# Kernel tuning notes

Measured on AMD Instinct MI355X. Metric: run time of the kernel, lower is better.

## Reference

```python
import jax, jax.numpy as jnp
import numpy as np

B = 256          # number of trees
DEPTH = 8        # complete binary tree depth -> 9 levels
M = 2 ** (DEPTH + 1) - 1   # 511 nodes per tree
N = B * M        # 130816 total nodes
X_SIZE = 128
H_SIZE = 128


def _build_forest():
    j = np.arange(M)
    parent_local = np.maximum((j - 1) // 2, 0)
    lvl = np.array([int(x + 1).bit_length() - 1 for x in j], dtype=np.int32)
    off = (np.arange(B) * M).astype(np.int32)
    parent = (parent_local[None, :] + off[:, None]).reshape(-1).astype(np.int32)
    level = np.tile(lvl, B)
    tree_id = np.repeat(np.arange(B, dtype=np.int32), M)
    isleaf = (level == DEPTH)
    jj = j[1:]
    edge_src = (jj[None, :] + off[:, None]).reshape(-1).astype(np.int32)   # child
    edge_dst = parent[edge_src]                                            # parent
    return parent, level, tree_id, isleaf, edge_src, edge_dst, off


def setup_inputs() -> dict:
    key = jax.random.key(0)
    ks = jax.random.split(key, 12)
    _, level, tree_id, isleaf, edge_src, edge_dst, root_ids = _build_forest()
    sx = 1.0 / np.sqrt(X_SIZE)
    sh = 1.0 / np.sqrt(H_SIZE)
    sxh = 1.0 / np.sqrt(X_SIZE + H_SIZE)
    inp = {
        "X": jax.random.normal(ks[0], (N, X_SIZE), dtype=jnp.float32),
        "h0": jnp.zeros((N, H_SIZE), jnp.float32),
        "c0": jnp.zeros((N, H_SIZE), jnp.float32),
        # bottom-up cell params
        "W_iou_bu": jax.random.normal(ks[1], (3 * H_SIZE, X_SIZE), dtype=jnp.float32) * sx,
        "U_iou_bu": jax.random.normal(ks[2], (3 * H_SIZE, H_SIZE), dtype=jnp.float32) * sh,
        "b_iou_bu": jnp.zeros((1, 3 * H_SIZE), jnp.float32),
        "Uf_bu": jax.random.normal(ks[3], (H_SIZE, H_SIZE), dtype=jnp.float32) * sh,
        "bf_bu": jax.random.normal(ks[4], (H_SIZE,), dtype=jnp.float32) * sh,
        # top-down cell params (x_size = X_SIZE + H_SIZE)
        "W_iou_td": jax.random.normal(ks[5], (3 * H_SIZE, X_SIZE + H_SIZE), dtype=jnp.float32) * sxh,
        "U_iou_td": jax.random.normal(ks[6], (3 * H_SIZE, H_SIZE), dtype=jnp.float32) * sh,
        "b_iou_td": jnp.zeros((1, 3 * H_SIZE), jnp.float32),
        "Uf_td": jax.random.normal(ks[7], (H_SIZE, H_SIZE), dtype=jnp.float32) * sh,
        "bf_td": jax.random.normal(ks[8], (H_SIZE,), dtype=jnp.float32) * sh,
        # graph structure
        "edge_src": jnp.asarray(edge_src),
        "edge_dst": jnp.asarray(edge_dst),
        "level": jnp.asarray(level),
        "tree_id": jnp.asarray(tree_id),
        "isleaf": jnp.asarray(isleaf),
        "root_ids": jnp.asarray(root_ids),
    }
    return inp


def _propagate(X_in, W_iou, U_iou, b_iou, Uf, bf, src, dst, level, no_in, h0, c0, order):
    """Level-synchronous ChildSum TreeLSTM propagation (== dgl.prop_nodes_topo)."""
    n = X_in.shape[0]
    WX = X_in @ W_iou.T                                   # [N, 3H]
    h, c = h0, c0
    for t in order:
        h_src = h[src]                                    # [E, H] gather child/parent states
        c_src = c[src]
        h_tild = jax.ops.segment_sum(h_src, dst, num_segments=n)
        f = jax.nn.sigmoid(h_src @ Uf.T + bf)             # per-edge forget gate
        c_red = jax.ops.segment_sum(f * c_src, dst, num_segments=n)
        iou = WX + h_tild @ U_iou.T + b_iou
        i, o, u = jnp.split(iou, 3, axis=1)
        c_base = jnp.where(no_in[:, None], c0, c_red)     # frontier nodes with no in-edges keep init c
        c_new = jax.nn.sigmoid(i) * jnp.tanh(u) + c_base
        h_new = jax.nn.sigmoid(o) * jnp.tanh(c_new)
        m = (level == t)[:, None]                          # only commit current topological level
        h = jnp.where(m, h_new, h)
        c = jnp.where(m, c_new, c)
    return h


def reference(X, h0, c0, W_iou_bu, U_iou_bu, b_iou_bu, Uf_bu, bf_bu,
              W_iou_td, U_iou_td, b_iou_td, Uf_td, bf_td,
              edge_src, edge_dst, level, tree_id, isleaf, root_ids):
    # bottom-up: messages flow child -> parent, leaves first
    h_bu = _propagate(X, W_iou_bu, U_iou_bu, b_iou_bu, Uf_bu, bf_bu,
                      edge_src, edge_dst, level, isleaf, h0, c0,
                      order=range(DEPTH, -1, -1))
    # top-down: reversed edges, root first
    X_td = jnp.concatenate([X, h_bu], axis=1)
    h_td = _propagate(X_td, W_iou_td, U_iou_td, b_iou_td, Uf_td, bf_td,
                      edge_dst, edge_src, level, level == 0, h0, c0,
                      order=range(0, DEPTH + 1))
    root_h_bottom_up = h_bu[root_ids]                     # [B, H]
    leaf = isleaf.astype(h_td.dtype)
    sums = jax.ops.segment_sum(h_td * leaf[:, None], tree_id, num_segments=root_ids.shape[0])
    cnt = jax.ops.segment_sum(leaf, tree_id, num_segments=root_ids.shape[0])
    leaves_h_top_down = sums / cnt[:, None]               # per-tree mean over leaves
    return jnp.concatenate([root_h_bottom_up, leaves_h_top_down], axis=1)
```

## Files before the change

kernel.cpp:

```cpp
#include <hip/hip_runtime.h>
#include <cmath>

#define NTREE 256
#define MPT 511
#define NNODE (NTREE * MPT)
#define HS 128

typedef __bf16 bf16x8 __attribute__((ext_vector_type(8)));
typedef float  f32x4  __attribute__((ext_vector_type(4)));

__device__ __forceinline__ float sigf(float x) {
  float e = __builtin_amdgcn_exp2f(x * -1.44269504f);
  return __builtin_amdgcn_rcpf(1.0f + e);
}
__device__ __forceinline__ float tanh_fast(float x) {
  float e = __builtin_amdgcn_exp2f(x * -2.88539008f);
  return __builtin_amdgcn_rcpf(1.0f + e) * 2.0f - 1.0f;
}
__device__ __forceinline__ f32x4 mm(bf16x8 a, bf16x8 b, f32x4 c) {
  return __builtin_amdgcn_mfma_f32_16x16x32_bf16(a, b, c, 0, 0, 0);
}
__device__ __forceinline__ int swz(int row, int rb, int kb) { return row * rb + (kb ^ ((row & 7) << 4)); }
__device__ __forceinline__ void st8(char* s, int row, int rb, int chunk, bf16x8 v) {
  *reinterpret_cast<bf16x8*>(s + swz(row, rb, chunk * 16)) = v;
}
__device__ __forceinline__ bf16x8 ld8(const char* s, int row, int rb, int kb) {
  return *reinterpret_cast<const bf16x8*>(s + swz(row, rb, kb));
}
__device__ __forceinline__ bf16x8 g8(const __bf16* p) { return *reinterpret_cast<const bf16x8*>(p); }
__device__ __forceinline__ bf16x8 gx8(const float* p) {
  float4 v0 = reinterpret_cast<const float4*>(p)[0];
  float4 v1 = reinterpret_cast<const float4*>(p)[1];
  bf16x8 o;
  o[0] = (__bf16)v0.x; o[1] = (__bf16)v0.y; o[2] = (__bf16)v0.z; o[3] = (__bf16)v0.w;
  o[4] = (__bf16)v1.x; o[5] = (__bf16)v1.y; o[6] = (__bf16)v1.z; o[7] = (__bf16)v1.w;
  return o;
}
__device__ __forceinline__ void stbf(char* s, int row, int rb, int kbyte, float v) {
  *reinterpret_cast<__bf16*>(s + row * rb + (kbyte ^ ((row & 7) << 4))) = (__bf16)v;
}

__global__ void __launch_bounds__(512, 2)
bu_bottom(const float* __restrict__ Xf,
          const __bf16* __restrict__ W, const float* __restrict__ bp,
          const __bf16* __restrict__ Uf, const float* __restrict__ bf_,
          __bf16* __restrict__ h_bu, float* __restrict__ cws)
{
  __shared__ __align__(16) char sX8[64 * 256];
  __shared__ __align__(16) char sX7[32 * 256];
  __shared__ __align__(16) char sT [32 * 256];
  __shared__ float sCr[32][128];

  const int tid = threadIdx.x, w = tid >> 6, l = tid & 63, lr = l & 15, lk = l >> 4;
  const int ch = w * 16 + lr;
  const int vb = blockIdx.x * 32;
  const int b  = vb >> 7;
  const int j7 = 127 + (vb & 127);
  const size_t g7  = (size_t)b * MPT + j7;
  const size_t gLf = (size_t)b * MPT + 2 * j7 + 1;
  const size_t gp6 = (size_t)b * MPT + ((j7 - 1) >> 1);

#pragma unroll
  for (int it = 0; it < 2; ++it) {
    int idx = tid + it * 512, n = idx >> 4, e = idx & 15;
    st8(sX8, n, 256, e, gx8(Xf + (gLf + n) * HS + e * 8));
  }
  { int n = tid >> 4, e = tid & 15;
    st8(sX7, n, 256, e, gx8(Xf + (g7 + n) * HS + e * 8)); }

  const float bia = bp[ch], boa = bp[ch + 128], bua = bp[ch + 256], bfa = bf_[ch];
  bf16x8 Uff[4];
#pragma unroll
  for (int ks = 0; ks < 4; ++ks) Uff[ks] = g8(Uf + (size_t)ch * HS + ks * 32 + lk * 8);
  __syncthreads();

  bf16x8 Bb[3][3];
  auto ldB = [&](int ks, int s) {
#pragma unroll
    for (int g2 = 0; g2 < 3; ++g2)
      Bb[s][g2] = g8(W + (size_t)(g2 * 128 + ch) * 256 + ks * 32 + lk * 8);
  };

  f32x4 acc[3][4];
#pragma unroll
  for (int g2 = 0; g2 < 3; ++g2)
#pragma unroll
    for (int mf = 0; mf < 4; ++mf) acc[g2][mf] = 0.0f;

  ldB(0, 0); ldB(1, 1);
#pragma unroll
  for (int ks = 0; ks < 4; ++ks) {
    if (ks + 2 < 4) ldB(ks + 2, (ks + 2) % 3);
    const int kb = ks * 64 + lk * 16;
    bf16x8 A0 = ld8(sX8, lr,      256, kb);
    bf16x8 A1 = ld8(sX8, 16 + lr, 256, kb);
    bf16x8 A2 = ld8(sX8, 32 + lr, 256, kb);
    bf16x8 A3 = ld8(sX8, 48 + lr, 256, kb);
#pragma unroll
    for (int g2 = 0; g2 < 3; ++g2) {
      acc[g2][0] = mm(A0, Bb[ks % 3][g2], acc[g2][0]);
      acc[g2][1] = mm(A1, Bb[ks % 3][g2], acc[g2][1]);
      acc[g2][2] = mm(A2, Bb[ks % 3][g2], acc[g2][2]);
      acc[g2][3] = mm(A3, Bb[ks % 3][g2], acc[g2][3]);
    }
  }
  float cnv[4][4], hnv[4][4];
#pragma unroll
  for (int mf = 0; mf < 4; ++mf)
#pragma unroll
    for (int j = 0; j < 4; ++j) {
      const int nrow = 16 * mf + lk * 4 + j;
      float cn = sigf(acc[0][mf][j] + bia) * tanh_fast(acc[2][mf][j] + bua);
      float hn = sigf(acc[1][mf][j] + boa) * tanh_fast(cn);
      cnv[mf][j] = cn; hnv[mf][j] = hn;
      h_bu[(gLf + nrow) * HS + ch] = (__bf16)hn;
    }
  __syncthreads();
#pragma unroll
  for (int mf = 0; mf < 4; ++mf)
#pragma unroll
    for (int j = 0; j < 4; ++j)
      stbf(sX8, 16 * mf + lk * 4 + j, 256, 2 * ch, hnv[mf][j]);
  __syncthreads();
  {
    f32x4 fa[4];
#pragma unroll
    for (int mf = 0; mf < 4; ++mf) fa[mf] = 0.0f;
#pragma unroll
    for (int ks = 0; ks < 4; ++ks) {
      const int kb = ks * 64 + lk * 16;
      fa[0] = mm(ld8(sX8, lr,      256, kb), Uff[ks], fa[0]);
      fa[1] = mm(ld8(sX8, 16 + lr, 256, kb), Uff[ks], fa[1]);
      fa[2] = mm(ld8(sX8, 32 + lr, 256, kb), Uff[ks], fa[2]);
      fa[3] = mm(ld8(sX8, 48 + lr, 256, kb), Uff[ks], fa[3]);
    }
#pragma unroll
    for (int mf = 0; mf < 4; ++mf)
#pragma unroll
      for (int p = 0; p < 2; ++p) {
        const int er = 16 * mf + lk * 4 + 2 * p;
        const int pr = er >> 1;
        float f0 = sigf(fa[mf][2 * p]     + bfa) * cnv[mf][2 * p];
        float f1 = sigf(fa[mf][2 * p + 1] + bfa) * cnv[mf][2 * p + 1];
        sCr[pr][ch] = f0 + f1;
        stbf(sT, pr, 256, 2 * ch, hnv[mf][2 * p] + hnv[mf][2 * p + 1]);
      }
  }
  __syncthreads();

  f32x4 ac2[3][2];
#pragma unroll
  for (int g2 = 0; g2 < 3; ++g2) { ac2[g2][0] = 0.0f; ac2[g2][1] = 0.0f; }
  ldB(0, 0); ldB(1, 1);
#pragma unroll
  for (int ks = 0; ks < 8; ++ks) {
    if (ks + 2 < 8) ldB(ks + 2, (ks + 2) % 3);
    const int kb = (ks & 3) * 64 + lk * 16;
    bf16x8 A0 = (ks < 4) ? ld8(sX7, lr,      256, kb) : ld8(sT, lr,      256, kb);
    bf16x8 A1 = (ks < 4) ? ld8(sX7, 16 + lr, 256, kb) : ld8(sT, 16 + lr, 256, kb);
#pragma unroll
    for (int g2 = 0; g2 < 3; ++g2) {
      ac2[g2][0] = mm(A0, Bb[ks % 3][g2], ac2[g2][0]);
      ac2[g2][1] = mm(A1, Bb[ks % 3][g2], ac2[g2][1]);
    }
  }
  float cn2[2][4], hn2[2][4];
#pragma unroll
  for (int mf = 0; mf < 2; ++mf)
#pragma unroll
    for (int j = 0; j < 4; ++j) {
      const int nr = 16 * mf + lk * 4 + j;
      float cn = sigf(ac2[0][mf][j] + bia) * tanh_fast(ac2[2][mf][j] + bua) + sCr[nr][ch];
      float hn = sigf(ac2[1][mf][j] + boa) * tanh_fast(cn);
      cn2[mf][j] = cn; hn2[mf][j] = hn;
      h_bu[(g7 + nr) * HS + ch] = (__bf16)hn;
    }
  __syncthreads();
#pragma unroll
  for (int mf = 0; mf < 2; ++mf)
#pragma unroll
    for (int j = 0; j < 4; ++j)
      stbf(sX7, 16 * mf + lk * 4 + j, 256, 2 * ch, hn2[mf][j]);
  __syncthreads();
  {
    f32x4 fb[2]; fb[0] = 0.0f; fb[1] = 0.0f;
#pragma unroll
    for (int ks = 0; ks < 4; ++ks) {
      const int kb = ks * 64 + lk * 16;
      fb[0] = mm(ld8(sX7, lr,      256, kb), Uff[ks], fb[0]);
      fb[1] = mm(ld8(sX7, 16 + lr, 256, kb), Uff[ks], fb[1]);
    }
#pragma unroll
    for (int mf = 0; mf < 2; ++mf)
#pragma unroll
      for (int p = 0; p < 2; ++p) {
        const int er = 16 * mf + lk * 4 + 2 * p;
        const size_t gp = gp6 + (er >> 1);
        float f0 = sigf(fb[mf][2 * p]     + bfa) * cn2[mf][2 * p];
        float f1 = sigf(fb[mf][2 * p + 1] + bfa) * cn2[mf][2 * p + 1];
        cws[gp * HS + ch] = f0 + f1;
        h_bu[gp * HS + ch] = (__bf16)(hn2[mf][2 * p] + hn2[mf][2 * p + 1]);
      }
  }
}

__global__ void __launch_bounds__(512, 2)
td_bottom(const float* __restrict__ Xf,
          const __bf16* __restrict__ W, const float* __restrict__ bp,
          const __bf16* __restrict__ Uf, const float* __restrict__ bf_,
          const __bf16* __restrict__ h_bu, const __bf16* __restrict__ h_td,
          const float* __restrict__ cws, float* __restrict__ part)
{
  __shared__ __align__(16) char sA7[32 * 768];
  __shared__ __align__(16) char sXH[64 * 512];
  __shared__ __align__(16) char sTd[32 * 256];
  __shared__ float sFc[32][128];

  const int tid = threadIdx.x, w = tid >> 6, l = tid & 63, lr = l & 15, lk = l >> 4;
  const int ch = w * 16 + lr;
  const int vb = blockIdx.x * 32;
  const int b  = vb >> 7;
  const int j7 = 127 + (vb & 127);
  const size_t g7  = (size_t)b * MPT + j7;
  const size_t gLf = (size_t)b * MPT + 2 * j7 + 1;
  const size_t gp6 = (size_t)b * MPT + ((j7 - 1) >> 1);

  { int n = tid >> 4, e = tid & 15;
    st8(sA7, n, 768, e,      gx8(Xf   + (g7 + n) * HS + e * 8));
    st8(sA7, n, 768, 16 + e, g8(h_bu + (g7 + n) * HS + e * 8));
    st8(sA7, n, 768, 32 + e, g8(h_td + (gp6 + (n >> 1)) * HS + e * 8)); }
#pragma unroll
  for (int it = 0; it < 2; ++it) {
    int idx = tid + it * 512, n = idx >> 4, e = idx & 15;
    st8(sXH, n, 512, e,      gx8(Xf   + (gLf + n) * HS + e * 8));
    st8(sXH, n, 512, 16 + e, g8(h_bu + (gLf + n) * HS + e * 8));
  }
  float cb[2][4];
#pragma unroll
  for (int mf = 0; mf < 2; ++mf)
#pragma unroll
    for (int j = 0; j < 4; ++j) {
      const int nr = 16 * mf + lk * 4 + j;
      cb[mf][j] = cws[(gp6 + (nr >> 1)) * HS + ch];
    }
  const float bia = bp[ch], boa = bp[ch + 128], bua = bp[ch + 256], bfa = bf_[ch];
  bf16x8 Uff[4];
#pragma unroll
  for (int ks = 0; ks < 4; ++ks) Uff[ks] = g8(Uf + (size_t)ch * HS + ks * 32 + lk * 8);
  __syncthreads();

  bf16x8 Bb[3][3];
  auto ldB = [&](int ks, int s) {
#pragma unroll
    for (int g2 = 0; g2 < 3; ++g2)
      Bb[s][g2] = g8(W + (size_t)(g2 * 128 + ch) * 384 + ks * 32 + lk * 8);
  };

  f32x4 ac[3][2];
#pragma unroll
  for (int g2 = 0; g2 < 3; ++g2) { ac[g2][0] = 0.0f; ac[g2][1] = 0.0f; }
  ldB(0, 0); ldB(1, 1);
#pragma unroll
  for (int ks = 0; ks < 12; ++ks) {
    if (ks + 2 < 12) ldB(ks + 2, (ks + 2) % 3);
    const int kb = ks * 64 + lk * 16;
    bf16x8 A0 = ld8(sA7, lr,      768, kb);
    bf16x8 A1 = ld8(sA7, 16 + lr, 768, kb);
#pragma unroll
    for (int g2 = 0; g2 < 3; ++g2) {
      ac[g2][0] = mm(A0, Bb[ks % 3][g2], ac[g2][0]);
      ac[g2][1] = mm(A1, Bb[ks % 3][g2], ac[g2][1]);
    }
  }
  float cn7[2][4];
#pragma unroll
  for (int mf = 0; mf < 2; ++mf)
#pragma unroll
    for (int j = 0; j < 4; ++j) {
      const int nr = 16 * mf + lk * 4 + j;
      float cn = sigf(ac[0][mf][j] + bia) * tanh_fast(ac[2][mf][j] + bua) + cb[mf][j];
      float hn = sigf(ac[1][mf][j] + boa) * tanh_fast(cn);
      cn7[mf][j] = cn;
      stbf(sTd, nr, 256, 2 * ch, hn);
    }
  __syncthreads();
  {
    f32x4 fa[2]; fa[0] = 0.0f; fa[1] = 0.0f;
#pragma unroll
    for (int ks = 0; ks < 4; ++ks) {
      const int kb = ks * 64 + lk * 16;
      fa[0] = mm(ld8(sTd, lr,      256, kb), Uff[ks], fa[0]);
      fa[1] = mm(ld8(sTd, 16 + lr, 256, kb), Uff[ks], fa[1]);
    }
#pragma unroll
    for (int mf = 0; mf < 2; ++mf)
#pragma unroll
      for (int j = 0; j < 4; ++j) {
        const int nr = 16 * mf + lk * 4 + j;
        sFc[nr][ch] = sigf(fa[mf][j] + bfa) * cn7[mf][j];
      }
  }
  __syncthreads();

  f32x4 a8[3][4];
#pragma unroll
  for (int g2 = 0; g2 < 3; ++g2)
#pragma unroll
    for (int mf = 0; mf < 4; ++mf) a8[g2][mf] = 0.0f;
  ldB(0, 0); ldB(1, 1);
#pragma unroll
  for (int ks = 0; ks < 12; ++ks) {
    if (ks + 2 < 12) ldB(ks + 2, (ks + 2) % 3);
    bf16x8 A0, A1, A2, A3;
    if (ks < 8) {
      const int kb = ks * 64 + lk * 16;
      A0 = ld8(sXH, lr,      512, kb);
      A1 = ld8(sXH, 16 + lr, 512, kb);
      A2 = ld8(sXH, 32 + lr, 512, kb);
      A3 = ld8(sXH, 48 + lr, 512, kb);
    } else {
      const int kb = (ks - 8) * 64 + lk * 16;
      A0 = ld8(sTd, (lr >> 1),      256, kb);
      A1 = ld8(sTd, 8 + (lr >> 1),  256, kb);
      A2 = ld8(sTd, 16 + (lr >> 1), 256, kb);
      A3 = ld8(sTd, 24 + (lr >> 1), 256, kb);
    }
#pragma unroll
    for (int g2 = 0; g2 < 3; ++g2) {
      a8[g2][0] = mm(A0, Bb[ks % 3][g2], a8[g2][0]);
      a8[g2][1] = mm(A1, Bb[ks % 3][g2], a8[g2][1]);
      a8[g2][2] = mm(A2, Bb[ks % 3][g2], a8[g2][2]);
      a8[g2][3] = mm(A3, Bb[ks % 3][g2], a8[g2][3]);
    }
  }
  float psum = 0.0f;
#pragma unroll
  for (int mf = 0; mf < 4; ++mf)
#pragma unroll
    for (int j = 0; j < 4; ++j) {
      const int nrow = 16 * mf + lk * 4 + j;
      float cbase = sFc[nrow >> 1][ch];
      float cn = sigf(a8[0][mf][j] + bia) * tanh_fast(a8[2][mf][j] + bua) + cbase;
      float hn = sigf(a8[1][mf][j] + boa) * tanh_fast(cn);
      psum += hn;
    }
  float s = psum;
  s += __shfl_xor(s, 16);
  s += __shfl_xor(s, 32);
  if (lk == 0) part[(size_t)blockIdx.x * 128 + ch] = s;
}

template <int MODE>
__global__ void __launch_bounds__(256, 2)
level_big(int t,
          const float*  __restrict__ Xf,
          const __bf16* __restrict__ W,
          const float*  __restrict__ bp,
          const __bf16* __restrict__ Uf,
          const float*  __restrict__ bf_,
          __bf16* __restrict__ h_bu,
          __bf16* __restrict__ h_td,
          float*  __restrict__ cws)
{
  constexpr int KA = (MODE == 1) ? 256 : 384;
  constexpr int KS = KA / 32;
  constexpr int BK = (MODE == 3) ? 384 : 256;
  constexpr int RB = KA * 2;
  constexpr int HB = (MODE == 1) ? 256 : 512;

  __shared__ __align__(16) char sA[64 * RB];
  __shared__ int sG[64], sP[64];

  const int tid = threadIdx.x;
  const int w = tid >> 6, l = tid & 63, lr = l & 15, lk = l >> 4;

  if (tid < 64) {
    int v = blockIdx.x * 64 + tid;
    int b = v >> t;
    int j = (1 << t) - 1 + (v & ((1 << t) - 1));
    sG[tid] = b * MPT + j;
    sP[tid] = b * MPT + ((j - 1) >> 1);
  }
  __syncthreads();

#pragma unroll
  for (int it = 0; it < 4; ++it) {
    int idx = tid + it * 256, n = idx >> 4, e = idx & 15;
    st8(sA, n, RB, e, gx8(Xf + (size_t)sG[n] * HS + e * 8));
  }
#pragma unroll
  for (int it = 0; it < 4; ++it) {
    int idx = tid + it * 256, n = idx >> 4, e = idx & 15;
    st8(sA, n, RB, 16 + e, g8(h_bu + (size_t)sG[n] * HS + e * 8));
  }
  if constexpr (MODE == 3) {
#pragma unroll
    for (int it = 0; it < 4; ++it) {
      int idx = tid + it * 256, n = idx >> 4, e = idx & 15;
      st8(sA, n, RB, 32 + e, g8(h_td + (size_t)sP[n] * HS + e * 8));
    }
  }
  __syncthreads();

  float cb[2][4][4];
  float bia[2], boa[2], bua[2], bfa[2];
#pragma unroll
  for (int nf = 0; nf < 2; ++nf) {
    const int ch = w * 32 + nf * 16 + lr;
    bia[nf] = bp[ch]; boa[nf] = bp[ch + 128]; bua[nf] = bp[ch + 256];
    bfa[nf] = bf_[ch];
#pragma unroll
    for (int mf = 0; mf < 4; ++mf)
#pragma unroll
      for (int j = 0; j < 4; ++j) {
        const int nrow = 16 * mf + lk * 4 + j;
        const int src = (MODE == 1) ? sG[nrow] : sP[nrow];
        cb[nf][mf][j] = cws[(size_t)src * HS + ch];
      }
  }

  f32x4 acc[6][4];
#pragma unroll
  for (int p = 0; p < 6; ++p)
#pragma unroll
    for (int mf = 0; mf < 4; ++mf) acc[p][mf] = 0.0f;

  bf16x8 A0[4], A1[4], Bb[3][6];
  auto ldA = [&](int ks, bf16x8* Ad) {
#pragma unroll
    for (int mf = 0; mf < 4; ++mf) Ad[mf] = ld8(sA, mf * 16 + lr, RB, ks * 64 + lk * 16);
  };
  auto ldB = [&](int ks, int s) {
#pragma unroll
    for (int g2 = 0; g2 < 3; ++g2)
#pragma unroll
      for (int nf = 0; nf < 2; ++nf)
        Bb[s][g2 * 2 + nf] = g8(W + (size_t)(g2 * 128 + w * 32 + nf * 16 + lr) * BK + ks * 32 + lk * 8);
  };

  ldB(0, 0); ldA(0, A0); ldB(1, 1);
#pragma unroll
  for (int ks = 0; ks < KS; ++ks) {
    bf16x8* Ac = (ks & 1) ? A1 : A0;
    bf16x8* An = (ks & 1) ? A0 : A1;
    if (ks + 1 < KS) ldA(ks + 1, An);
    if (ks + 2 < KS) ldB(ks + 2, (ks + 2) % 3);
#pragma unroll
    for (int p = 0; p < 6; ++p)
#pragma unroll
      for (int mf = 0; mf < 4; ++mf) acc[p][mf] = mm(Ac[mf], Bb[ks % 3][p], acc[p][mf]);
  }

  bf16x8 Uff[8];
#pragma unroll
  for (int ks = 0; ks < 4; ++ks)
#pragma unroll
    for (int nf = 0; nf < 2; ++nf)
      Uff[ks * 2 + nf] = g8(Uf + (size_t)(w * 32 + nf * 16 + lr) * HS + ks * 32 + lk * 8);

  __bf16* hp = (MODE == 3) ? h_td : h_bu;
  float cnv[2][4][4], hnv[2][4][4];
#pragma unroll
  for (int nf = 0; nf < 2; ++nf) {
    const int ch = w * 32 + nf * 16 + lr;
#pragma unroll
    for (int mf = 0; mf < 4; ++mf)
#pragma unroll
      for (int j = 0; j < 4; ++j) {
        const int nrow = 16 * mf + lk * 4 + j;
        float cn = sigf(acc[nf][mf][j] + bia[nf]) * tanh_fast(acc[4 + nf][mf][j] + bua[nf]) + cb[nf][mf][j];
        float hn = sigf(acc[2 + nf][mf][j] + boa[nf]) * tanh_fast(cn);
        hp[(size_t)sG[nrow] * HS + ch] = (__bf16)hn;
        cnv[nf][mf][j] = cn; hnv[nf][mf][j] = hn;
      }
  }

  __syncthreads();
#pragma unroll
  for (int nf = 0; nf < 2; ++nf) {
    const int ch = w * 32 + nf * 16 + lr;
#pragma unroll
    for (int mf = 0; mf < 4; ++mf)
#pragma unroll
      for (int j = 0; j < 4; ++j)
        stbf(sA, 16 * mf + lk * 4 + j, RB, HB + 2 * ch, hnv[nf][mf][j]);
  }
  __syncthreads();
  f32x4 fa[4][2];
#pragma unroll
  for (int mf = 0; mf < 4; ++mf) { fa[mf][0] = 0.0f; fa[mf][1] = 0.0f; }
#pragma unroll
  for (int ks = 0; ks < 4; ++ks) {
    bf16x8 a0 = ld8(sA, lr,      RB, HB + ks * 64 + lk * 16);
    bf16x8 a1 = ld8(sA, 16 + lr, RB, HB + ks * 64 + lk * 16);
    bf16x8 a2 = ld8(sA, 32 + lr, RB, HB + ks * 64 + lk * 16);
    bf16x8 a3 = ld8(sA, 48 + lr, RB, HB + ks * 64 + lk * 16);
#pragma unroll
    for (int nf = 0; nf < 2; ++nf) {
      fa[0][nf] = mm(a0, Uff[ks * 2 + nf], fa[0][nf]);
      fa[1][nf] = mm(a1, Uff[ks * 2 + nf], fa[1][nf]);
      fa[2][nf] = mm(a2, Uff[ks * 2 + nf], fa[2][nf]);
      fa[3][nf] = mm(a3, Uff[ks * 2 + nf], fa[3][nf]);
    }
  }
#pragma unroll
  for (int nf = 0; nf < 2; ++nf) {
    const int ch = w * 32 + nf * 16 + lr;
    if constexpr (MODE == 3) {
#pragma unroll
      for (int mf = 0; mf < 4; ++mf)
#pragma unroll
        for (int j = 0; j < 4; ++j) {
          const int nrow = 16 * mf + lk * 4 + j;
          cws[(size_t)sG[nrow] * HS + ch] = sigf(fa[mf][nf][j] + bfa[nf]) * cnv[nf][mf][j];
        }
    } else {
#pragma unroll
      for (int mf = 0; mf < 4; ++mf)
#pragma unroll
        for (int p = 0; p < 2; ++p) {
          const int er = 16 * mf + lk * 4 + 2 * p;
          float f0 = sigf(fa[mf][nf][2 * p]     + bfa[nf]) * cnv[nf][mf][2 * p];
          float f1 = sigf(fa[mf][nf][2 * p + 1] + bfa[nf]) * cnv[nf][mf][2 * p + 1];
          const int gp = sP[er];
          cws[(size_t)gp * HS + ch] = f0 + f1;
          h_bu[(size_t)gp * HS + ch] = (__bf16)(hnv[nf][mf][2 * p] + hnv[nf][mf][2 * p + 1]);
        }
    }
  }
}

__global__ void __launch_bounds__(512, 2)
small_both(const float* __restrict__ Xf,
           const __bf16* __restrict__ Wbu, const float* __restrict__ bbu,
           const __bf16* __restrict__ Ufb, const float* __restrict__ bfb,
           const __bf16* __restrict__ Wtd, const float* __restrict__ btd,
           const __bf16* __restrict__ Uft, const float* __restrict__ bft,
           __bf16* __restrict__ h_bu, __bf16* __restrict__ h_td,
           float* __restrict__ cws)
{
  __shared__ __align__(16) char sX[31 * 256];
  __shared__ __align__(16) char sH[31 * 256];
  __shared__ __align__(16) char sT[16 * 256];
  __shared__ __align__(16) char sTd[15 * 256];
  __shared__ float sCr[16][128];
  __shared__ float sFc[16][128];

  const int tid = threadIdx.x, w = tid >> 6, l = tid & 63, lr = l & 15, lk = l >> 4;
  const int ch = w * 16 + lr;
  const size_t base = (size_t)blockIdx.x * MPT * HS;

  for (int idx = tid; idx < 31 * 16; idx += 512) {
    int n = idx >> 4, e = idx & 15;
    st8(sX, n, 256, e, gx8(Xf + base + (size_t)n * HS + e * 8));
  }
  if (tid < 256) { int n = tid >> 4, e = tid & 15;
    st8(sT, n, 256, e, g8(h_bu + base + (size_t)(15 + n) * HS + e * 8)); }
  { int n = tid >> 5, e = tid & 31;
    reinterpret_cast<float4*>(&sCr[n][0])[e] =
        reinterpret_cast<const float4*>(cws + base + (size_t)(15 + n) * HS)[e]; }
  for (int idx = tid; idx < 15 * 16; idx += 512)
    *reinterpret_cast<float4*>(sTd + idx * 16) = float4{0.f, 0.f, 0.f, 0.f};

  {
    const float bia = bbu[ch], boa = bbu[ch + 128], bua = bbu[ch + 256], bfa = bfb[ch];
    bf16x8 Wb[8][3], Uff[4];
#pragma unroll
    for (int ks = 0; ks < 8; ++ks)
#pragma unroll
      for (int g2 = 0; g2 < 3; ++g2)
        Wb[ks][g2] = g8(Wbu + (size_t)(g2 * 128 + ch) * 256 + ks * 32 + lk * 8);
#pragma unroll
    for (int ks = 0; ks < 4; ++ks)
      Uff[ks] = g8(Ufb + (size_t)ch * HS + ks * 32 + lk * 8);
    __syncthreads();

    for (int t = 4; t >= 0; --t) {
      const int cnt = 1 << t, j0 = cnt - 1;
      f32x4 acc0 = 0.0f, acc1 = 0.0f, acc2 = 0.0f;
      bf16x8 Aa[3];
      auto ldA = [&](int ks, int s) {
        const int kb = (ks & 3) * 64 + lk * 16;
        Aa[s] = (ks < 4) ? ld8(sX, j0 + lr, 256, kb) : ld8(sT, lr, 256, kb);
      };
      ldA(0, 0); ldA(1, 1);
#pragma unroll
      for (int ks = 0; ks < 8; ++ks) {
        if (ks + 2 < 8) ldA(ks + 2, (ks + 2) % 3);
        acc0 = mm(Aa[ks % 3], Wb[ks][0], acc0);
        acc1 = mm(Aa[ks % 3], Wb[ks][1], acc1);
        acc2 = mm(Aa[ks % 3], Wb[ks][2], acc2);
      }
      float cnv[4], hnv[4];
#pragma unroll
      for (int j = 0; j < 4; ++j) {
        const int r = lk * 4 + j;
        float cn = sigf(acc0[j] + bia) * tanh_fast(acc2[j] + bua) + sCr[r][ch];
        float hn = sigf(acc1[j] + boa) * tanh_fast(cn);
        cnv[j] = cn; hnv[j] = hn;
        if (r < cnt) stbf(sH, j0 + r, 256, 2 * ch, hn);
      }
      if (t == 0 && lk == 0) h_bu[base + ch] = (__bf16)hnv[0];
      __syncthreads();
      if (t > 0) {
        f32x4 fa = 0.0f;
#pragma unroll
        for (int ks = 0; ks < 4; ++ks)
          fa = mm(ld8(sH, j0 + lr, 256, ks * 64 + lk * 16), Uff[ks], fa);
#pragma unroll
        for (int p = 0; p < 2; ++p) {
          const int pr = lk * 2 + p;
          if (pr < (cnt >> 1)) {
            float f0 = sigf(fa[2 * p]     + bfa) * cnv[2 * p];
            float f1 = sigf(fa[2 * p + 1] + bfa) * cnv[2 * p + 1];
            sCr[pr][ch] = f0 + f1;
            stbf(sT, pr, 256, 2 * ch, hnv[2 * p] + hnv[2 * p + 1]);
          }
        }
      }
      __syncthreads();
    }
  }

  {
    const float bia = btd[ch], boa = btd[ch + 128], bua = btd[ch + 256], bfa = bft[ch];
    bf16x8 Wt[12][3], Uff[4];
#pragma unroll
    for (int ks = 0; ks < 12; ++ks)
#pragma unroll
      for (int g2 = 0; g2 < 3; ++g2)
        Wt[ks][g2] = g8(Wtd + (size_t)(g2 * 128 + ch) * 384 + ks * 32 + lk * 8);
#pragma unroll
    for (int ks = 0; ks < 4; ++ks)
      Uff[ks] = g8(Uft + (size_t)ch * HS + ks * 32 + lk * 8);

    for (int t = 0; t <= 4; ++t) {
      const int cnt = 1 << t, j0 = cnt - 1;
      f32x4 acc0 = 0.0f, acc1 = 0.0f, acc2 = 0.0f;
      bf16x8 Aa[3];
      auto ldA = [&](int ks, int s) {
        const int kb = (ks & 3) * 64 + lk * 16;
        if (ks < 4)      Aa[s] = ld8(sX, j0 + lr, 256, kb);
        else if (ks < 8) Aa[s] = ld8(sH, j0 + lr, 256, kb);
        else { int pr = (j0 + lr - 1) >> 1; pr = pr < 0 ? 0 : pr;
               Aa[s] = ld8(sTd, pr, 256, kb); }
      };
      ldA(0, 0); ldA(1, 1);
#pragma unroll
      for (int ks = 0; ks < 12; ++ks) {
        if (ks + 2 < 12) ldA(ks + 2, (ks + 2) % 3);
        acc0 = mm(Aa[ks % 3], Wt[ks][0], acc0);
        acc1 = mm(Aa[ks % 3], Wt[ks][1], acc1);
        acc2 = mm(Aa[ks % 3], Wt[ks][2], acc2);
      }
      float cnv[4], hnv[4];
#pragma unroll
      for (int j = 0; j < 4; ++j) {
        const int r = lk * 4 + j;
        float cbv = (t == 0) ? 0.0f : sFc[r >> 1][ch];
        float cn = sigf(acc0[j] + bia) * tanh_fast(acc2[j] + bua) + cbv;
        float hn = sigf(acc1[j] + boa) * tanh_fast(cn);
        cnv[j] = cn; hnv[j] = hn;
        stbf(sT, r, 256, 2 * ch, hn);
        if (r < cnt && j0 + r < 15) stbf(sTd, j0 + r, 256, 2 * ch, hn);
        if (t == 4) h_td[base + (size_t)(15 + r) * HS + ch] = (__bf16)hn;
      }
      __syncthreads();
      f32x4 fa = 0.0f;
#pragma unroll
      for (int ks = 0; ks < 4; ++ks)
        fa = mm(ld8(sT, lr, 256, ks * 64 + lk * 16), Uff[ks], fa);
#pragma unroll
      for (int j = 0; j < 4; ++j) {
        const int r = lk * 4 + j;
        float fcv = sigf(fa[j] + bfa) * cnv[j];
        if (r < cnt) {
          if (t < 4) sFc[r][ch] = fcv;
          else       cws[base + (size_t)(15 + r) * HS + ch] = fcv;
        }
      }
      __syncthreads();
    }
  }
}

__global__ void __launch_bounds__(256)
prep(const float* __restrict__ Wbu, const float* __restrict__ Ubu,
     const float* __restrict__ Wtd, const float* __restrict__ Utd,
     const float* __restrict__ Ufb, const float* __restrict__ Uft,
     __bf16* wbu, __bf16* wtd, __bf16* ufb, __bf16* uft)
{
  int i = blockIdx.x * 256 + threadIdx.x;
  if (i < 98304) {
    int r = i >> 8, c = i & 255;
    wbu[i] = (__bf16)(c < 128 ? Wbu[r * 128 + c] : Ubu[r * 128 + c - 128]);
  } else if (i < 245760) {
    int k = i - 98304; int r = k / 384, c = k - r * 384;
    wtd[k] = (__bf16)(c < 256 ? Wtd[r * 256 + c] : Utd[r * 128 + (c - 256)]);
  } else if (i < 262144) {
    int k = i - 245760; ufb[k] = (__bf16)Ufb[k];
  } else {
    int k = i - 262144; uft[k] = (__bf16)Uft[k];
  }
}

__global__ void __launch_bounds__(128)
finalize_kernel(const __bf16* __restrict__ h_bu, const float* __restrict__ part,
                float* __restrict__ out)
{
  int b = blockIdx.x, ch = threadIdx.x;
  out[(size_t)b * 256 + ch] = (float)h_bu[((size_t)b * MPT) * HS + ch];
  const float* pp = part + (size_t)b * 512 + ch;
  out[(size_t)b * 256 + 128 + ch] = (pp[0] + pp[128] + pp[256] + pp[384]) * (1.0f / 256.0f);
}

extern "C" void kernel_launch(void* const* d_in, const int* in_sizes, int n_in,
                              void* d_out, int out_size, void* d_ws, size_t ws_size,
                              hipStream_t stream) {
  const float* X     = (const float*)d_in[0];
  const float* W_bu  = (const float*)d_in[3];
  const float* U_bu  = (const float*)d_in[4];
  const float* b_bu  = (const float*)d_in[5];
  const float* Uf_bu = (const float*)d_in[6];
  const float* bf_bu = (const float*)d_in[7];
  const float* W_td  = (const float*)d_in[8];
  const float* U_td  = (const float*)d_in[9];
  const float* b_td  = (const float*)d_in[10];
  const float* Uf_td = (const float*)d_in[11];
  const float* bf_td = (const float*)d_in[12];

  char* p = (char*)d_ws;
  __bf16* wbu  = (__bf16*)p; p += (size_t)384 * 256 * 2;
  __bf16* wtd  = (__bf16*)p; p += (size_t)384 * 384 * 2;
  __bf16* ufb  = (__bf16*)p; p += (size_t)128 * 128 * 2;
  __bf16* uft  = (__bf16*)p; p += (size_t)128 * 128 * 2;
  __bf16* h_bu = (__bf16*)p; p += (size_t)NNODE * HS * 2;
  __bf16* h_td = (__bf16*)p; p += (size_t)NNODE * HS * 2;
  float*  cws  = (float*)p;  p += (size_t)NNODE * HS * 4;
  float*  part = (float*)p;

  prep<<<1088, 256, 0, stream>>>(W_bu, U_bu, W_td, U_td, Uf_bu, Uf_td, wbu, wtd, ufb, uft);

  bu_bottom<<<1024, 512, 0, stream>>>(X, wbu, b_bu, ufb, bf_bu, h_bu, cws);
  level_big<1><<<256, 256, 0, stream>>>(6, X, wbu, b_bu, ufb, bf_bu, h_bu, h_td, cws);
  level_big<1><<<128, 256, 0, stream>>>(5, X, wbu, b_bu, ufb, bf_bu, h_bu, h_td, cws);

  small_both<<<256, 512, 0, stream>>>(X, wbu, b_bu, ufb, bf_bu,
                                      wtd, b_td, uft, bf_td, h_bu, h_td, cws);

  level_big<3><<<128, 256, 0, stream>>>(5, X, wtd, b_td, uft, bf_td, h_bu, h_td, cws);
  level_big<3><<<256, 256, 0, stream>>>(6, X, wtd, b_td, uft, bf_td, h_bu, h_td, cws);
  td_bottom<<<1024, 512, 0, stream>>>(X, wtd, b_td, uft, bf_td, h_bu, h_td, cws, part);

  finalize_kernel<<<256, 128, 0, stream>>>(h_bu, part, (float*)d_out);
}
```

Measured before the change: 260.1 us.

## Keep full gate weight fragments register-resident in bottom kernels, drop occupancy to one

In bu_bottom and td_bottom, the whole per-lane gate weight slice (8 or 12 k-steps × 3 gates) is now loaded into registers once at kernel start. The triple-buffered streaming loads that re-fetched the same weights in each of the two GEMM phases are gone. Launch bounds drop from 2 to 1 block per CU so the compiler can hold the extra VGPRs. This halves global weight traffic per block and overlaps the weight loads with the X staging, at the cost of lower occupancy and less latency hiding.

```diff
diff --git a/kernel.cpp b/kernel.cpp
--- a/kernel.cpp
+++ b/kernel.cpp
@@ -40,7 +40,7 @@
   *reinterpret_cast<__bf16*>(s + row * rb + (kbyte ^ ((row & 7) << 4))) = (__bf16)v;
 }
 
-__global__ void __launch_bounds__(512, 2)
+__global__ void __launch_bounds__(512, 1)
 bu_bottom(const float* __restrict__ Xf,
           const __bf16* __restrict__ W, const float* __restrict__ bp,
           const __bf16* __restrict__ Uf, const float* __restrict__ bf_,
@@ -60,6 +60,15 @@
   const size_t gLf = (size_t)b * MPT + 2 * j7 + 1;
   const size_t gp6 = (size_t)b * MPT + ((j7 - 1) >> 1);
 
+  bf16x8 Wb[8][3], Uff[4];
+#pragma unroll
+  for (int ks = 0; ks < 8; ++ks)
+#pragma unroll
+    for (int g2 = 0; g2 < 3; ++g2)
+      Wb[ks][g2] = g8(W + (size_t)(g2 * 128 + ch) * 256 + ks * 32 + lk * 8);
+#pragma unroll
+  for (int ks = 0; ks < 4; ++ks) Uff[ks] = g8(Uf + (size_t)ch * HS + ks * 32 + lk * 8);
+
 #pragma unroll
   for (int it = 0; it < 2; ++it) {
     int idx = tid + it * 512, n = idx >> 4, e = idx & 15;
@@ -69,17 +78,7 @@
     st8(sX7, n, 256, e, gx8(Xf + (g7 + n) * HS + e * 8)); }
 
   const float bia = bp[ch], boa = bp[ch + 128], bua = bp[ch + 256], bfa = bf_[ch];
-  bf16x8 Uff[4];
-#pragma unroll
-  for (int ks = 0; ks < 4; ++ks) Uff[ks] = g8(Uf + (size_t)ch * HS + ks * 32 + lk * 8);
-  __syncthreads();
-
-  bf16x8 Bb[3][3];
-  auto ldB = [&](int ks, int s) {
-#pragma unroll
-    for (int g2 = 0; g2 < 3; ++g2)
-      Bb[s][g2] = g8(W + (size_t)(g2 * 128 + ch) * 256 + ks * 32 + lk * 8);
-  };
+  __syncthreads();
 
   f32x4 acc[3][4];
 #pragma unroll
@@ -87,10 +86,8 @@
 #pragma unroll
     for (int mf = 0; mf < 4; ++mf) acc[g2][mf] = 0.0f;
 
-  ldB(0, 0); ldB(1, 1);
 #pragma unroll
   for (int ks = 0; ks < 4; ++ks) {
-    if (ks + 2 < 4) ldB(ks + 2, (ks + 2) % 3);
     const int kb = ks * 64 + lk * 16;
     bf16x8 A0 = ld8(sX8, lr,      256, kb);
     bf16x8 A1 = ld8(sX8, 16 + lr, 256, kb);
@@ -98,10 +95,10 @@
     bf16x8 A3 = ld8(sX8, 48 + lr, 256, kb);
 #pragma unroll
     for (int g2 = 0; g2 < 3; ++g2) {
-      acc[g2][0] = mm(A0, Bb[ks % 3][g2], acc[g2][0]);
-      acc[g2][1] = mm(A1, Bb[ks % 3][g2], acc[g2][1]);
-      acc[g2][2] = mm(A2, Bb[ks % 3][g2], acc[g2][2]);
-      acc[g2][3] = mm(A3, Bb[ks % 3][g2], acc[g2][3]);
+      acc[g2][0] = mm(A0, Wb[ks][g2], acc[g2][0]);
+      acc[g2][1] = mm(A1, Wb[ks][g2], acc[g2][1]);
+      acc[g2][2] = mm(A2, Wb[ks][g2], acc[g2][2]);
+      acc[g2][3] = mm(A3, Wb[ks][g2], acc[g2][3]);
     }
   }
   float cnv[4][4], hnv[4][4];
@@ -151,17 +148,15 @@
   f32x4 ac2[3][2];
 #pragma unroll
   for (int g2 = 0; g2 < 3; ++g2) { ac2[g2][0] = 0.0f; ac2[g2][1] = 0.0f; }
-  ldB(0, 0); ldB(1, 1);
 #pragma unroll
   for (int ks = 0; ks < 8; ++ks) {
-    if (ks + 2 < 8) ldB(ks + 2, (ks + 2) % 3);
     const int kb = (ks & 3) * 64 + lk * 16;
     bf16x8 A0 = (ks < 4) ? ld8(sX7, lr,      256, kb) : ld8(sT, lr,      256, kb);
     bf16x8 A1 = (ks < 4) ? ld8(sX7, 16 + lr, 256, kb) : ld8(sT, 16 + lr, 256, kb);
 #pragma unroll
     for (int g2 = 0; g2 < 3; ++g2) {
-      ac2[g2][0] = mm(A0, Bb[ks % 3][g2], ac2[g2][0]);
-      ac2[g2][1] = mm(A1, Bb[ks % 3][g2], ac2[g2][1]);
+      ac2[g2][0] = mm(A0, Wb[ks][g2], ac2[g2][0]);
+      ac2[g2][1] = mm(A1, Wb[ks][g2], ac2[g2][1]);
     }
   }
   float cn2[2][4], hn2[2][4];
@@ -204,7 +199,7 @@
   }
 }
 
-__global__ void __launch_bounds__(512, 2)
+__global__ void __launch_bounds__(512, 1)
 td_bottom(const float* __restrict__ Xf,
           const __bf16* __restrict__ W, const float* __restrict__ bp,
           const __bf16* __restrict__ Uf, const float* __restrict__ bf_,
@@ -225,6 +220,15 @@
   const size_t gLf = (size_t)b * MPT + 2 * j7 + 1;
   const size_t gp6 = (size_t)b * MPT + ((j7 - 1) >> 1);
 
+  bf16x8 Wt[12][3], Uff[4];
+#pragma unroll
+  for (int ks = 0; ks < 12; ++ks)
+#pragma unroll
+    for (int g2 = 0; g2 < 3; ++g2)
+      Wt[ks][g2] = g8(W + (size_t)(g2 * 128 + ch) * 384 + ks * 32 + lk * 8);
+#pragma unroll
+  for (int ks = 0; ks < 4; ++ks) Uff[ks] = g8(Uf + (size_t)ch * HS + ks * 32 + lk * 8);
+
   { int n = tid >> 4, e = tid & 15;
     st8(sA7, n, 768, e,      gx8(Xf   + (g7 + n) * HS + e * 8));
     st8(sA7, n, 768, 16 + e, g8(h_bu + (g7 + n) * HS + e * 8));
@@ -244,32 +248,20 @@
       cb[mf][j] = cws[(gp6 + (nr >> 1)) * HS + ch];
     }
   const float bia = bp[ch], boa = bp[ch + 128], bua = bp[ch + 256], bfa = bf_[ch];
-  bf16x8 Uff[4];
-#pragma unroll
-  for (int ks = 0; ks < 4; ++ks) Uff[ks] = g8(Uf + (size_t)ch * HS + ks * 32 + lk * 8);
-  __syncthreads();
-
-  bf16x8 Bb[3][3];
-  auto ldB = [&](int ks, int s) {
-#pragma unroll
-    for (int g2 = 0; g2 < 3; ++g2)
-      Bb[s][g2] = g8(W + (size_t)(g2 * 128 + ch) * 384 + ks * 32 + lk * 8);
-  };
+  __syncthreads();
 
   f32x4 ac[3][2];
 #pragma unroll
   for (int g2 = 0; g2 < 3; ++g2) { ac[g2][0] = 0.0f; ac[g2][1] = 0.0f; }
-  ldB(0, 0); ldB(1, 1);
 #pragma unroll
   for (int ks = 0; ks < 12; ++ks) {
-    if (ks + 2 < 12) ldB(ks + 2, (ks + 2) % 3);
     const int kb = ks * 64 + lk * 16;
     bf16x8 A0 = ld8(sA7, lr,      768, kb);
     bf16x8 A1 = ld8(sA7, 16 + lr, 768, kb);
 #pragma unroll
     for (int g2 = 0; g2 < 3; ++g2) {
-      ac[g2][0] = mm(A0, Bb[ks % 3][g2], ac[g2][0]);
-      ac[g2][1] = mm(A1, Bb[ks % 3][g2], ac[g2][1]);
+      ac[g2][0] = mm(A0, Wt[ks][g2], ac[g2][0]);
+      ac[g2][1] = mm(A1, Wt[ks][g2], ac[g2][1]);
     }
   }
   float cn7[2][4];
@@ -307,10 +299,8 @@
   for (int g2 = 0; g2 < 3; ++g2)
 #pragma unroll
     for (int mf = 0; mf < 4; ++mf) a8[g2][mf] = 0.0f;
-  ldB(0, 0); ldB(1, 1);
 #pragma unroll
   for (int ks = 0; ks < 12; ++ks) {
-    if (ks + 2 < 12) ldB(ks + 2, (ks + 2) % 3);
     bf16x8 A0, A1, A2, A3;
     if (ks < 8) {
       const int kb = ks * 64 + lk * 16;
@@ -327,10 +317,10 @@
     }
 #pragma unroll
     for (int g2 = 0; g2 < 3; ++g2) {
-      a8[g2][0] = mm(A0, Bb[ks % 3][g2], a8[g2][0]);
-      a8[g2][1] = mm(A1, Bb[ks % 3][g2], a8[g2][1]);
-      a8[g2][2] = mm(A2, Bb[ks % 3][g2], a8[g2][2]);
-      a8[g2][3] = mm(A3, Bb[ks % 3][g2], a8[g2][3]);
+      a8[g2][0] = mm(A0, Wt[ks][g2], a8[g2][0]);
+      a8[g2][1] = mm(A1, Wt[ks][g2], a8[g2][1]);
+      a8[g2][2] = mm(A2, Wt[ks][g2], a8[g2][2]);
+      a8[g2][3] = mm(A3, Wt[ks][g2], a8[g2][3]);
     }
   }
   float psum = 0.0f;
```

Result: faster. 237.2 us (-8.8%).
